# Performance work log

Measured on AMD Instinct MI355X. Metric: run time of the kernel, lower is better.

## Reference

```python
import jax, jax.numpy as jnp
import numpy as np

EPS = 1e-6
NUM_HEADS = 8
GAMMA = 0.999


def simple_rms_norm(x):
    # SimpleRMSNorm: x / ||x|| * sqrt(d) == x / sqrt(mean(x^2))
    return x * jax.lax.rsqrt(jnp.mean(x * x, axis=-1, keepdims=True) + EPS)


def setup_inputs() -> dict:
    key = jax.random.key(0)
    ks = jax.random.split(key, 12)
    B, N, M, E = 64, 14, 14, 512
    D1 = 2 * E              # expand_ratio * embed_dim = 1024
    RPE = 512               # rpe_embedding
    s = 0.02
    inp = {
        "x": jax.random.normal(ks[0], (B, N, M, E), jnp.float32),
        "H": N,
        "W": M,
        "Wu": jax.random.normal(ks[1], (E, D1), jnp.float32) * s,
        "bu": jnp.zeros((D1,), jnp.float32),
        "Wv": jax.random.normal(ks[2], (E, D1), jnp.float32) * s,
        "bv": jnp.zeros((D1,), jnp.float32),
        "Wo": jax.random.normal(ks[3], (D1, E), jnp.float32) * s,
        "bo": jnp.zeros((E,), jnp.float32),
        "rpe_pos_w": jax.random.normal(ks[4], (2, RPE), jnp.float32) * s,
        "rpe_pos_b": jnp.zeros((RPE,), jnp.float32),
        "rpe_w1": jax.random.normal(ks[5], (RPE, RPE), jnp.float32) * s,
        "rpe_b1": jnp.zeros((RPE,), jnp.float32),
        "rpe_w2": jax.random.normal(ks[6], (RPE, RPE), jnp.float32) * s,
        "rpe_b2": jnp.zeros((RPE,), jnp.float32),
        "rpe_w3": jax.random.normal(ks[7], (RPE, RPE), jnp.float32) * s,
        "rpe_b3": jnp.zeros((RPE,), jnp.float32),
        "rpe_out_w": jax.random.normal(ks[8], (RPE, D1), jnp.float32) * s,
        "rpe_out_b": jnp.zeros((D1,), jnp.float32),
    }
    return inp


def gtu2d_forward(x, Wu, bu, Wv, bv, Wo, bo,
                  rpe_pos_w, rpe_pos_b, rpe_w1, rpe_b1, rpe_w2, rpe_b2,
                  rpe_w3, rpe_b3, rpe_out_w, rpe_out_b):
    B, n, m, E = x.shape
    d1 = Wu.shape[1]
    hd = d1 // NUM_HEADS
    # dual gated projections
    u = jax.nn.silu(x @ Wu + bu)                      # (B, n, m, d1)
    v = jax.nn.silu(x @ Wv + bv)
    v = v.reshape(B, n, m, NUM_HEADS, hd).transpose(0, 3, 1, 2, 4)  # (B, h, n, m, d)

    # --- Tno2D: RPE MLP produces Toeplitz coefficients for relative positions ---
    ii = jnp.arange(-(n - 1), n, dtype=jnp.float32)
    jj = jnp.arange(-(m - 1), m, dtype=jnp.float32)
    pos = jnp.stack(jnp.meshgrid(ii, jj, indexing="ij"), axis=-1)  # (2n-1, 2m-1, 2)
    r = pos @ rpe_pos_w + rpe_pos_b
    for w, b in ((rpe_w1, rpe_b1), (rpe_w2, rpe_b2), (rpe_w3, rpe_b3)):
        r = jax.nn.relu(simple_rms_norm(r)) @ w + b
    r = jax.nn.relu(simple_rms_norm(r)) @ rpe_out_w + rpe_out_b  # (2n-1, 2m-1, h*d)
    a = r.reshape(2 * n - 1, 2 * m - 1, NUM_HEADS, hd).transpose(2, 0, 1, 3)
    # decay: gamma^(|i|+|j|)
    dist = jnp.abs(pos[..., 0]) + jnp.abs(pos[..., 1])  # (2n-1, 2m-1)
    a = a * (GAMMA ** dist)[None, :, :, None]

    # embed coefficients into circular kernel (h, 2n, 2m, d); index n / m are zero
    t = jnp.zeros((NUM_HEADS, 2 * n, 2 * m, hd), a.dtype)
    t = t.at[:, :n, :m].set(a[:, n - 1:, m - 1:])
    t = t.at[:, n + 1:, :m].set(a[:, :n - 1, m - 1:])
    t = t.at[:, :n, m + 1:].set(a[:, n - 1:, :m - 1])
    t = t.at[:, n + 1:, m + 1:].set(a[:, :n - 1, :m - 1])

    # 2D Toeplitz matvec via circular convolution / FFT
    xf = jnp.fft.rfft2(v, s=(2 * n, 2 * m), axes=(2, 3))
    tf = jnp.fft.rfft2(t, s=(2 * n, 2 * m), axes=(1, 2))
    y = jnp.fft.irfft2(xf * tf[None], s=(2 * n, 2 * m), axes=(2, 3))[:, :, :n, :m, :]
    y = y.transpose(0, 2, 3, 1, 4).reshape(B, n, m, d1)  # 'b h n m d -> b n m (h d)'

    return (u * y) @ Wo + bo


def reference(x, H, W, Wu, bu, Wv, bv, Wo, bo,
              rpe_pos_w, rpe_pos_b, rpe_w1, rpe_b1, rpe_w2, rpe_b2,
              rpe_w3, rpe_b3, rpe_out_w, rpe_out_b):
    # H, W are unused by Gtu2d.forward (spatial dims are carried by x)
    return gtu2d_forward(x, Wu, bu, Wv, bv, Wo, bo,
                         rpe_pos_w, rpe_pos_b, rpe_w1, rpe_b1, rpe_w2, rpe_b2,
                         rpe_w3, rpe_b3, rpe_out_w, rpe_out_b)
```

## Files before the change

kernel.cpp:

```cpp
#include <hip/hip_runtime.h>
#include <hip/hip_bf16.h>

typedef __hip_bfloat16 bf16;
typedef __attribute__((ext_vector_type(8))) short bf16x8;
typedef __attribute__((ext_vector_type(4))) float f32x4;

constexpr int NB    = 64;
constexpr int EE    = 512;
constexpr int RPOS  = 27 * 27;
constexpr int ROWS  = NB * 14 * 14;
constexpr int UVNWG = 392;

#define RMS_EPS 1e-6f
#define GAMMA_LOG2 (-0.00144344319f)

__device__ __forceinline__ void  stf(float* p, float v) { *p = v; }
__device__ __forceinline__ void  stf(bf16* p, float v)  { *p = __float2bfloat16(v); }

__device__ __forceinline__ void gload_lds16(const bf16* g, bf16* l) {
    __builtin_amdgcn_global_load_lds(
        (const __attribute__((address_space(1))) void*)g,
        (__attribute__((address_space(3))) void*)l, 16, 0, 0);
}

#define VMCNT(n) asm volatile("s_waitcnt vmcnt(" #n ")" ::: "memory")

__global__ __launch_bounds__(256) void k_prep(const float* __restrict__ Wu,
                                              const float* __restrict__ Wv,
                                              const float* __restrict__ Wo,
                                              const float* __restrict__ w1,
                                              const float* __restrict__ w2,
                                              const float* __restrict__ w3,
                                              const float* __restrict__ wOut,
                                              const float* __restrict__ bu,
                                              const float* __restrict__ bv,
                                              const float* __restrict__ x,
                                              const float* __restrict__ rpw,
                                              const float* __restrict__ rpb,
                                              bf16* __restrict__ WuvT,
                                              bf16* __restrict__ WoT,
                                              bf16* __restrict__ w1T,
                                              bf16* __restrict__ w2T,
                                              bf16* __restrict__ w3T,
                                              bf16* __restrict__ wOutT,
                                              float* __restrict__ biasUv,
                                              bf16* __restrict__ xb,
                                              bf16* __restrict__ rnA) {
    __shared__ float t[32][33];
    __shared__ float ps[4];
    const int tid = threadIdx.x;
    int b = blockIdx.x;

    const float* src = nullptr; bf16* dst = nullptr; int R = 0, C = 0, nbx = 0;
    if (b < 512)        { src = Wu;   dst = WuvT;                      R = 512;  C = 1024; nbx = 32; }
    else if (b < 1024)  { b -= 512;   src = Wv; dst = WuvT + (size_t)1024 * 512; R = 512; C = 1024; nbx = 32; }
    else if (b < 1536)  { b -= 1024;  src = Wo;   dst = WoT;           R = 1024; C = 512;  nbx = 16; }
    else if (b < 1792)  { b -= 1536;  src = w1;   dst = w1T;           R = 512;  C = 512;  nbx = 16; }
    else if (b < 2048)  { b -= 1792;  src = w2;   dst = w2T;           R = 512;  C = 512;  nbx = 16; }
    else if (b < 2304)  { b -= 2048;  src = w3;   dst = w3T;           R = 512;  C = 512;  nbx = 16; }
    else if (b < 2816)  { b -= 2304;  src = wOut; dst = wOutT;         R = 512;  C = 1024; nbx = 32; }
    else if (b < 2824) {
        int c = (b - 2816) * 256 + tid;
        if (c < 2048) biasUv[c] = (c < 1024) ? bu[c] : bv[c - 1024];
        return;
    } else if (b < 9096) {
        int i = (b - 2824) * 256 + tid;
        float4 v = *(const float4*)&x[(size_t)i * 4];
        bf16* d = &xb[(size_t)i * 4];
        d[0] = __float2bfloat16(v.x);
        d[1] = __float2bfloat16(v.y);
        d[2] = __float2bfloat16(v.z);
        d[3] = __float2bfloat16(v.w);
        return;
    } else {
        int p = b - 9096;
        float ii = (float)(p / 27 - 13);
        float jj = (float)(p % 27 - 13);
        int c0 = tid, c1 = tid + 256;
        float v0 = ii * rpw[c0] + jj * rpw[512 + c0] + rpb[c0];
        float v1 = ii * rpw[c1] + jj * rpw[512 + c1] + rpb[c1];
        float s = v0 * v0 + v1 * v1;
        #pragma unroll
        for (int off = 32; off; off >>= 1) s += __shfl_down(s, off, 64);
        if ((tid & 63) == 0) ps[tid >> 6] = s;
        __syncthreads();
        float tot = ps[0] + ps[1] + ps[2] + ps[3];
        float scale = rsqrtf(tot * (1.0f / 512.0f) + RMS_EPS);
        rnA[(size_t)p * 512 + c0] = __float2bfloat16(fmaxf(v0 * scale, 0.0f));
        rnA[(size_t)p * 512 + c1] = __float2bfloat16(fmaxf(v1 * scale, 0.0f));
        return;
    }
    int bx = (b % nbx) * 32;
    int by = (b / nbx) * 32;
    int tx = tid & 31, ty = tid >> 5;
    #pragma unroll
    for (int i = 0; i < 4; ++i)
        t[ty + i * 8][tx] = src[(size_t)(by + ty + i * 8) * C + bx + tx];
    __syncthreads();
    #pragma unroll
    for (int i = 0; i < 4; ++i)
        dst[(size_t)(bx + ty + i * 8) * R + by + tx] = __float2bfloat16(t[tx][ty + i * 8]);
}

template <int SCALE_IN, int EPI>
__device__ __forceinline__ void rpe_body(const bf16* __restrict__ A,
                                         const bf16* __restrict__ Bt,
                                         const float* __restrict__ bias,
                                         const float* __restrict__ pIn,
                                         float* __restrict__ pOut,
                                         bf16* __restrict__ out,
                                         int bx, int by, int M, int N, int K,
                                         bf16* As, bf16* Bs, int tid) {
    const int m0 = by * 64;
    const int n0 = bx * 64;
    const int lane = tid & 63;
    const int w = (tid >> 6) & 3;
    const int lr = lane & 15;
    const int lk = (lane >> 4) * 8;
    const int row = tid >> 2;
    const int seg = (tid & 3) * 8;

    f32x4 acc[4] = {};
    const int KT = K >> 5;

    gload_lds16(&A[(size_t)(m0 + row) * K + seg], &As[tid * 8]);
    gload_lds16(&Bt[(size_t)(n0 + row) * K + seg], &Bs[tid * 8]);
    for (int t = 0; t < KT; ++t) {
        const int d = t & 1;
        if (t + 1 < KT) {
            gload_lds16(&A[(size_t)(m0 + row) * K + (t + 1) * 32 + seg], &As[(d ^ 1) * 2048 + tid * 8]);
            gload_lds16(&Bt[(size_t)(n0 + row) * K + (t + 1) * 32 + seg], &Bs[(d ^ 1) * 2048 + tid * 8]);
            VMCNT(2);
        } else {
            VMCNT(0);
        }
        __builtin_amdgcn_s_barrier();
        __builtin_amdgcn_sched_barrier(0);
        bf16x8 af = *(const bf16x8*)&As[d * 2048 + (w * 16 + lr) * 32 + lk];
        #pragma unroll
        for (int j = 0; j < 4; ++j) {
            bf16x8 bf = *(const bf16x8*)&Bs[d * 2048 + (j * 16 + lr) * 32 + lk];
            acc[j] = __builtin_amdgcn_mfma_f32_16x16x32_bf16(af, bf, acc[j], 0, 0, 0);
        }
        __builtin_amdgcn_s_barrier();
    }

    const int crow = (lane >> 4) * 4;
    const int ccol = lane & 15;
    float sc[4];
    #pragma unroll
    for (int r = 0; r < 4; ++r) {
        sc[r] = 1.0f;
        if (SCALE_IN) {
            int gr = m0 + w * 16 + crow + r;
            if (gr < M) {
                const float* pp = &pIn[(size_t)gr * 8];
                float s8 = pp[0] + pp[1] + pp[2] + pp[3] + pp[4] + pp[5] + pp[6] + pp[7];
                sc[r] = rsqrtf(s8 * (1.0f / 512.0f) + RMS_EPS);
            }
        }
    }
    float rowsq[4] = {0.f, 0.f, 0.f, 0.f};
    #pragma unroll
    for (int j = 0; j < 4; ++j) {
        int gc = n0 + j * 16 + ccol;
        float bb = bias[gc];
        #pragma unroll
        for (int r = 0; r < 4; ++r) {
            int gr = m0 + w * 16 + crow + r;
            float val = acc[j][r] * sc[r] + bb;
            if (EPI == 0) {
                rowsq[r] += val * val;
                if (gr < M) out[(size_t)gr * N + gc] = __float2bfloat16(fmaxf(val, 0.0f));
            } else {
                if (gr < M) {
                    int i = gr / 27, jj = gr % 27;
                    float decay = exp2f((float)(abs(i - 13) + abs(jj - 13)) * GAMMA_LOG2);
                    out[(size_t)gr * N + gc] = __float2bfloat16(val * decay);
                }
            }
        }
    }
    if (EPI == 0) {
        #pragma unroll
        for (int r = 0; r < 4; ++r) {
            #pragma unroll
            for (int m = 1; m < 16; m <<= 1) rowsq[r] += __shfl_xor(rowsq[r], m, 64);
        }
        if ((lane & 15) == 0) {
            #pragma unroll
            for (int r = 0; r < 4; ++r) {
                int gr = m0 + w * 16 + crow + r;
                if (gr < M) pOut[(size_t)gr * 8 + bx] = rowsq[r];
            }
        }
    }
}

template <int SCALE_IN, int EPI>
__global__ __launch_bounds__(256) void k_rpe_gemm(const bf16* __restrict__ A,
                                                  const bf16* __restrict__ Bt,
                                                  const float* __restrict__ bias,
                                                  const float* __restrict__ pIn,
                                                  float* __restrict__ pOut,
                                                  bf16* __restrict__ out,
                                                  int M, int N, int K) {
    __shared__ bf16 As[2][2048];
    __shared__ bf16 Bs[2][2048];
    rpe_body<SCALE_IN, EPI>(A, Bt, bias, pIn, pOut, out,
                            blockIdx.x, blockIdx.y, M, N, K,
                            &As[0][0], &Bs[0][0], threadIdx.x);
}

template <int EPI, typename TO>
__global__ __launch_bounds__(256) void k_mgemm(const bf16* __restrict__ A, int lda,
                                               const bf16* __restrict__ Bt,
                                               const float* __restrict__ bias,
                                               TO* __restrict__ out, int ldo,
                                               int M, int N, int K) {
    __shared__ bf16 As[128 * 32];
    __shared__ bf16 Bs[128 * 32];
    const int tid = threadIdx.x;
    const int m0 = blockIdx.y * 128;
    const int n0 = blockIdx.x * 128;
    const int lane = tid & 63;
    const int w = tid >> 6;
    const int wr = (w >> 1) * 64;
    const int wc = (w & 1) * 64;
    const int lr = lane & 15;
    const int lk = (lane >> 4) * 8;

    f32x4 acc[4][4] = {};

    for (int k0 = 0; k0 < K; k0 += 32) {
        #pragma unroll
        for (int t = 0; t < 2; ++t) {
            int flat = t * 256 + tid;
            int row = flat >> 2;
            int seg = (flat & 3) * 8;
            gload_lds16(&A[(size_t)(m0 + row) * lda + k0 + seg], &As[flat * 8]);
            gload_lds16(&Bt[(size_t)(n0 + row) * K + k0 + seg], &Bs[flat * 8]);
        }
        __syncthreads();
        bf16x8 af[4], bf[4];
        #pragma unroll
        for (int i = 0; i < 4; ++i) {
            af[i] = *(const bf16x8*)&As[(wr + i * 16 + lr) * 32 + lk];
            bf[i] = *(const bf16x8*)&Bs[(wc + i * 16 + lr) * 32 + lk];
        }
        #pragma unroll
        for (int i = 0; i < 4; ++i)
            #pragma unroll
            for (int j = 0; j < 4; ++j)
                acc[i][j] = __builtin_amdgcn_mfma_f32_16x16x32_bf16(af[i], bf[j], acc[i][j], 0, 0, 0);
        __syncthreads();
    }

    const int crow = (lane >> 4) * 4;
    const int ccol = lane & 15;
    #pragma unroll
    for (int i = 0; i < 4; ++i)
        #pragma unroll
        for (int j = 0; j < 4; ++j) {
            int gc = n0 + wc + j * 16 + ccol;
            float bb = bias[gc];
            #pragma unroll
            for (int r = 0; r < 4; ++r) {
                int gr = m0 + wr + i * 16 + crow + r;
                float val = acc[i][j][r] + bb;
                if (EPI == 1) val = val / (1.0f + expf(-val));
                stf(&out[(size_t)gr * ldo + gc], val);
            }
        }
}

__global__ __launch_bounds__(512, 2) void k_uv_l1(const bf16* __restrict__ A, int lda,
                                                  const bf16* __restrict__ Bt,
                                                  const float* __restrict__ bias,
                                                  bf16* __restrict__ out, int ldo,
                                                  int nb ,
                                                  const bf16* __restrict__ rA,
                                                  const bf16* __restrict__ w1T,
                                                  const float* __restrict__ b1,
                                                  float* __restrict__ p1,
                                                  bf16* __restrict__ rB) {
    constexpr int KT = 8;
    constexpr int K = KT * 64;
    __shared__ __align__(16) char lds[131072];

    const int tid = threadIdx.x;

    if (blockIdx.x >= UVNWG) {
        const int orig = (blockIdx.x - UVNWG) * 2 + (tid >> 8);
        const int half = tid >> 8;
        bf16* As = (bf16*)(lds + half * 32768);
        bf16* Bs = (bf16*)(lds + half * 32768 + 8192);
        rpe_body<0, 0>(rA, w1T, b1, nullptr, p1, rB,
                       orig & 7, orig >> 3, RPOS, 512, 512, As, Bs, tid & 255);
        return;
    }

    const int lane = tid & 63;
    const int wid = tid >> 6;
    const int wr = wid >> 2;
    const int wc = wid & 3;

    int wgid = blockIdx.x;
    {
        int cpx = UVNWG >> 3;
        wgid = (wgid & 7) * cpx + (wgid >> 3);
    }
    const int m0 = (wgid / nb) * 256;
    const int n0 = (wgid % nb) * 256;

    auto ldsA = [&](int d, int kh) -> char* { return (char*)lds + d * 32768 + kh * 16384; };
    auto ldsB = [&](int d, int kh) -> char* { return (char*)lds + 65536 + d * 32768 + kh * 16384; };

    auto stage = [&](int op, int kh, int tt) {
        char* base = op ? ldsB(tt & 1, kh) : ldsA(tt & 1, kh);
        const bf16* g = op ? Bt : A;
        const int rowbase = op ? n0 : m0;
        const int ldr = op ? K : lda;
        #pragma unroll
        for (int l = 0; l < 2; ++l) {
            int q = tid + l * 512;
            int r = q >> 2;
            int cl = (q & 3) ^ ((r ^ (r >> 2)) & 3);
            const bf16* src = g + (size_t)(rowbase + r) * ldr + tt * 64 + kh * 32 + cl * 8;
            gload_lds16(src, (bf16*)(base + q * 16));
        }
    };
    auto rdA = [&](int d, int ks, int mi) -> bf16x8 {
        int row = wr * 128 + mi * 16 + (lane & 15);
        int ch = (lane >> 4) ^ ((row ^ (row >> 2)) & 3);
        return *(const bf16x8*)(ldsA(d, ks) + row * 64 + ch * 16);
    };
    auto rdB = [&](int d, int ks, int nj) -> bf16x8 {
        int row = wc * 64 + nj * 16 + (lane & 15);
        int ch = (lane >> 4) ^ ((row ^ (row >> 2)) & 3);
        return *(const bf16x8*)(ldsB(d, ks) + row * 64 + ch * 16);
    };

    f32x4 acc[8][4] = {};
    bf16x8 aF[4], bF[4];

    stage(0, 0, 0); stage(1, 0, 0); stage(0, 1, 0); stage(1, 1, 0);
    stage(0, 0, 1); stage(1, 0, 1);
    VMCNT(8);
    __builtin_amdgcn_s_barrier();
    __builtin_amdgcn_sched_barrier(0);

    #pragma unroll
    for (int t = 0; t < KT; ++t) {
        const int d = t & 1;
        #pragma unroll
        for (int mi = 0; mi < 4; ++mi) aF[mi] = rdA(d, 0, mi);
        #pragma unroll
        for (int nj = 0; nj < 4; ++nj) bF[nj] = rdB(d, 0, nj);
        if (t + 1 < KT) stage(0, 1, t + 1);
        __builtin_amdgcn_s_barrier();
        __builtin_amdgcn_s_setprio(1);
        #pragma unroll
        for (int mi = 0; mi < 4; ++mi)
            #pragma unroll
            for (int nj = 0; nj < 4; ++nj)
                acc[mi][nj] = __builtin_amdgcn_mfma_f32_16x16x32_bf16(aF[mi], bF[nj], acc[mi][nj], 0, 0, 0);
        __builtin_amdgcn_s_setprio(0);
        __builtin_amdgcn_s_barrier();
        #pragma unroll
        for (int mi = 0; mi < 4; ++mi) aF[mi] = rdA(d, 0, mi + 4);
        if (t + 1 < KT) stage(1, 1, t + 1);
        if (t + 1 < KT) { VMCNT(8); } else { VMCNT(0); }
        __builtin_amdgcn_s_barrier();
        __builtin_amdgcn_sched_barrier(0);
        __builtin_amdgcn_s_setprio(1);
        #pragma unroll
        for (int mi = 0; mi < 4; ++mi)
            #pragma unroll
            for (int nj = 0; nj < 4; ++nj)
                acc[mi + 4][nj] = __builtin_amdgcn_mfma_f32_16x16x32_bf16(aF[mi], bF[nj], acc[mi + 4][nj], 0, 0, 0);
        __builtin_amdgcn_s_setprio(0);
        __builtin_amdgcn_s_barrier();
        #pragma unroll
        for (int mi = 0; mi < 4; ++mi) aF[mi] = rdA(d, 1, mi);
        #pragma unroll
        for (int nj = 0; nj < 4; ++nj) bF[nj] = rdB(d, 1, nj);
        if (t + 2 < KT) stage(0, 0, t + 2);
        __builtin_amdgcn_s_barrier();
        __builtin_amdgcn_s_setprio(1);
        #pragma unroll
        for (int mi = 0; mi < 4; ++mi)
            #pragma unroll
            for (int nj = 0; nj < 4; ++nj)
                acc[mi][nj] = __builtin_amdgcn_mfma_f32_16x16x32_bf16(aF[mi], bF[nj], acc[mi][nj], 0, 0, 0);
        __builtin_amdgcn_s_setprio(0);
        __builtin_amdgcn_s_barrier();
        #pragma unroll
        for (int mi = 0; mi < 4; ++mi) aF[mi] = rdA(d, 1, mi + 4);
        if (t + 2 < KT) stage(1, 0, t + 2);
        if (t + 2 < KT)      { VMCNT(8); }
        else if (t + 1 < KT) { VMCNT(4); }
        __builtin_amdgcn_s_barrier();
        __builtin_amdgcn_sched_barrier(0);
        __builtin_amdgcn_s_setprio(1);
        #pragma unroll
        for (int mi = 0; mi < 4; ++mi)
            #pragma unroll
            for (int nj = 0; nj < 4; ++nj)
                acc[mi + 4][nj] = __builtin_amdgcn_mfma_f32_16x16x32_bf16(aF[mi], bF[nj], acc[mi + 4][nj], 0, 0, 0);
        __builtin_amdgcn_s_setprio(0);
        __builtin_amdgcn_s_barrier();
    }

    const int crow = (lane >> 4) * 4;
    const int ccol = lane & 15;
    #pragma unroll
    for (int mi = 0; mi < 8; ++mi)
        #pragma unroll
        for (int nj = 0; nj < 4; ++nj) {
            int gc = n0 + wc * 64 + nj * 16 + ccol;
            float bb = bias[gc];
            #pragma unroll
            for (int r = 0; r < 4; ++r) {
                int gr = m0 + wr * 128 + mi * 16 + crow + r;
                float val = acc[mi][nj][r] + bb;
                val = val / (1.0f + expf(-val));
                stf(&out[(size_t)gr * ldo + gc], val);
            }
        }
}

__global__ __launch_bounds__(256) void k_vt_l2(const bf16* __restrict__ uv,
                                               bf16* __restrict__ Vt,
                                               const bf16* __restrict__ rB,
                                               const bf16* __restrict__ w2T,
                                               const float* __restrict__ b2,
                                               const float* __restrict__ p1,
                                               float* __restrict__ p2,
                                               bf16* __restrict__ rA) {
    __shared__ __align__(16) char lraw[25872 > 16384 ? 25872 : 16384];
    const int tid = threadIdx.x;

    if (blockIdx.x >= 1024) {
        const int orig = blockIdx.x - 1024;
        bf16* As = (bf16*)lraw;
        bf16* Bs = (bf16*)(lraw + 8192);
        rpe_body<1, 0>(rB, w2T, b2, p1, p2, rA,
                       orig & 7, orig >> 3, RPOS, 512, 512, As, Bs, tid);
        return;
    }

    typedef bf16 row66[66];
    row66* t = (row66*)lraw;
    const int c0 = (blockIdx.x & 15) * 64;
    const int b  = blockIdx.x >> 4;
    for (int f = tid; f < 196 * 64; f += 256) {
        int ij = f >> 6, cl = f & 63;
        t[ij][cl] = uv[((size_t)b * 196 + ij) * 2048 + 1024 + c0 + cl];
    }
    __syncthreads();
    const bf16 z = __float2bfloat16(0.0f);
    for (int f = tid; f < 64 * 224; f += 256) {
        int cl = f / 224, ij = f - cl * 224;
        Vt[((size_t)(c0 + cl) * 64 + b) * 224 + ij] = (ij < 196) ? t[ij][cl] : z;
    }
}

__global__ __launch_bounds__(256) void k_convm(const bf16* __restrict__ Ab,
                                               const bf16* __restrict__ Vt,
                                               bf16* __restrict__ Yt) {
    __shared__ __align__(16) bf16 Ts[112 * 232];
    __shared__ bf16 As[736];
    const int mh = blockIdx.x;
    const int cl = blockIdx.y;
    const int c = (int)blockIdx.z * 512 + cl;
    const int tid = threadIdx.x;
    const int mbase = mh * 112;

    for (int e = tid; e < 729; e += 256)
        As[e] = Ab[(size_t)e * 1024 + c];
    __syncthreads();

    const bf16 z = __float2bfloat16(0.0f);
    if (tid < 224) {
        const int i = tid / 14, j = tid - i * 14;
        const bool kvalid = tid < 196;
        int p = mbase / 14, q = 0;
        for (int r = 0; r < 112; ++r) {
            bf16 val = z;
            if (kvalid && (mbase + r) < 196)
                val = As[(p - i + 13) * 27 + (q - j + 13)];
            Ts[r * 232 + tid] = val;
            if (++q == 14) { q = 0; ++p; }
        }
    }
    __syncthreads();

    const int lane = tid & 63;
    const int w = tid >> 6;
    const int lr = lane & 15;
    const int lk = (lane >> 4) * 8;
    const bf16* Vc = Vt + (size_t)c * 64 * 224;

    bf16x8 bfr[7];
    #pragma unroll
    for (int ks = 0; ks < 7; ++ks)
        bfr[ks] = *(const bf16x8*)&Vc[(size_t)(w * 16 + lr) * 224 + ks * 32 + lk];

    f32x4 acc[7] = {};
    #pragma unroll
    for (int ks = 0; ks < 7; ++ks)
        #pragma unroll
        for (int mi = 0; mi < 7; ++mi) {
            bf16x8 a = *(const bf16x8*)&Ts[(mi * 16 + lr) * 232 + ks * 32 + lk];
            acc[mi] = __builtin_amdgcn_mfma_f32_16x16x32_bf16(a, bfr[ks], acc[mi], 0, 0, 0);
        }

    const int crow = (lane >> 4) * 4;
    const int bb = w * 16 + (lane & 15);
    #pragma unroll
    for (int mi = 0; mi < 7; ++mi) {
        int pq = mbase + mi * 16 + crow;
        #pragma unroll
        for (int r = 0; r < 4; ++r)
            if (pq + r < 196)
                Yt[((size_t)c * 196 + pq + r) * 64 + bb] = __float2bfloat16(acc[mi][r]);
    }
}

__global__ __launch_bounds__(256) void k_gate(bf16* __restrict__ uv,
                                              const bf16* __restrict__ Yt) {
    const int pq = blockIdx.x;
    const int ct = blockIdx.y;
    const int cb = (int)blockIdx.z * 512;
    const int tid = threadIdx.x;
    __shared__ float t[64][65];
    for (int f = tid; f < 64 * 64; f += 256) {
        int cr = f >> 6, bcol = f & 63;
        t[cr][bcol] = __bfloat162float(Yt[((size_t)(cb + ct * 64 + cr) * 196 + pq) * 64 + bcol]);
    }
    __syncthreads();
    for (int f = tid; f < 64 * 64; f += 256) {
        int br = f >> 6, cc = f & 63;
        size_t row = (size_t)br * 196 + pq;
        int cglob = cb + ct * 64 + cc;
        float uu = __bfloat162float(uv[row * 2048 + cglob]);
        uv[row * 2048 + 1024 + cglob] = __float2bfloat16(t[cc][br] * uu);
    }
}

extern "C" void kernel_launch(void* const* d_in, const int* in_sizes, int n_in,
                              void* d_out, int out_size, void* d_ws, size_t ws_size,
                              hipStream_t stream) {
    const float* x    = (const float*)d_in[0];
    const float* Wu   = (const float*)d_in[3];
    const float* bu   = (const float*)d_in[4];
    const float* Wv   = (const float*)d_in[5];
    const float* bv   = (const float*)d_in[6];
    const float* Wo   = (const float*)d_in[7];
    const float* bo   = (const float*)d_in[8];
    const float* rpw  = (const float*)d_in[9];
    const float* rpb  = (const float*)d_in[10];
    const float* w1   = (const float*)d_in[11];
    const float* b1   = (const float*)d_in[12];
    const float* w2   = (const float*)d_in[13];
    const float* b2   = (const float*)d_in[14];
    const float* w3   = (const float*)d_in[15];
    const float* b3   = (const float*)d_in[16];
    const float* wOut = (const float*)d_in[17];
    const float* bOut = (const float*)d_in[18];

    char* ws = (char*)d_ws;
    size_t off = 0;
    auto take = [&](size_t bytes) { char* p = ws + off; off += (bytes + 255) & ~size_t(255); return p; };
    bf16*  rnA    = (bf16*)take((size_t)768 * 512 * 2);
    bf16*  rnB    = (bf16*)take((size_t)768 * 512 * 2);
    float* p1     = (float*)take((size_t)768 * 8 * 4);
    float* p2     = (float*)take((size_t)768 * 8 * 4);
    float* p3     = (float*)take((size_t)768 * 8 * 4);
    bf16*  Ab     = (bf16*)take((size_t)RPOS * 1024 * 2);
    bf16*  xb     = (bf16*)take((size_t)ROWS * EE * 2);
    bf16*  WuvT   = (bf16*)take((size_t)2048 * 512 * 2);
    bf16*  WoT    = (bf16*)take((size_t)512 * 1024 * 2);
    bf16*  w1T    = (bf16*)take((size_t)512 * 512 * 2);
    bf16*  w2T    = (bf16*)take((size_t)512 * 512 * 2);
    bf16*  w3T    = (bf16*)take((size_t)512 * 512 * 2);
    bf16*  wOutT  = (bf16*)take((size_t)1024 * 512 * 2);
    float* biasUv = (float*)take(2048 * 4);
    bf16*  uvb    = (bf16*)take((size_t)ROWS * 2048 * 2);
    bf16*  Vt     = (bf16*)take((size_t)1024 * 64 * 224 * 2);
    bf16*  Yt     = (bf16*)take((size_t)1024 * 196 * 64 * 2);

    k_prep<<<9825, 256, 0, stream>>>(Wu, Wv, Wo, w1, w2, w3, wOut, bu, bv, x,
                                     rpw, rpb,
                                     WuvT, WoT, w1T, w2T, w3T, wOutT, biasUv, xb, rnA);

    k_uv_l1<<<UVNWG + 48, 512, 0, stream>>>(xb, 512, WuvT, biasUv, uvb, 2048, 8,
                                            rnA, w1T, b1, p1, rnB);

    k_vt_l2<<<1120, 256, 0, stream>>>(uvb, Vt, rnB, w2T, b2, p1, p2, rnA);

    k_rpe_gemm<1, 0><<<dim3(8, 12), 256, 0, stream>>>(rnA, w3T, b3, p2, p3, rnB, RPOS, 512, 512);
    k_rpe_gemm<1, 2><<<dim3(16, 12), 256, 0, stream>>>(rnB, wOutT, bOut, p3, nullptr, Ab, RPOS, 1024, 512);

    k_convm<<<dim3(2, 512, 2), 256, 0, stream>>>(Ab, Vt, Yt);
    k_gate<<<dim3(196, 8, 2), 256, 0, stream>>>(uvb, Yt);

    k_mgemm<0, float><<<dim3(4, 98), 256, 0, stream>>>(uvb + 1024, 2048, WoT, bo,
                                                       (float*)d_out, 512, ROWS, 512, 1024);
}
```

Measured before the change: 198.3 us.

## Split V transpose across two launches co-scheduled with RPE layers 2 and 3

The V-transpose work is split into two halves by batch. Each half is fused with one RPE MLP layer (layer 2 and then layer 3), which removes the standalone layer-3 RPE GEMM launch and lets the small RPE GEMMs overlap with the memory-bound transpose. Separately, the conv kernel now processes both 112-row halves in one block, loading the Toeplitz coefficients and V fragments once instead of twice. This halves the grid and adds an extra barrier round per block, which reduces parallelism in exchange for reuse.

```diff
diff --git a/kernel.cpp b/kernel.cpp
--- a/kernel.cpp
+++ b/kernel.cpp
@@ -430,22 +430,22 @@
         }
 }
 
-__global__ __launch_bounds__(256) void k_vt_l2(const bf16* __restrict__ uv,
-                                               bf16* __restrict__ Vt,
-                                               const bf16* __restrict__ rB,
-                                               const bf16* __restrict__ w2T,
-                                               const float* __restrict__ b2,
-                                               const float* __restrict__ p1,
-                                               float* __restrict__ p2,
-                                               bf16* __restrict__ rA) {
-    __shared__ __align__(16) char lraw[25872 > 16384 ? 25872 : 16384];
+__global__ __launch_bounds__(256) void k_vt_rpe(const bf16* __restrict__ uv,
+                                                bf16* __restrict__ Vt, int bbase,
+                                                const bf16* __restrict__ rIn,
+                                                const bf16* __restrict__ wT,
+                                                const float* __restrict__ bias,
+                                                const float* __restrict__ pIn,
+                                                float* __restrict__ pOut,
+                                                bf16* __restrict__ rOut) {
+    __shared__ __align__(16) char lraw[25872];
     const int tid = threadIdx.x;
 
-    if (blockIdx.x >= 1024) {
-        const int orig = blockIdx.x - 1024;
+    if (blockIdx.x >= 512) {
+        const int orig = blockIdx.x - 512;
         bf16* As = (bf16*)lraw;
         bf16* Bs = (bf16*)(lraw + 8192);
-        rpe_body<1, 0>(rB, w2T, b2, p1, p2, rA,
+        rpe_body<1, 0>(rIn, wT, bias, pIn, pOut, rOut,
                        orig & 7, orig >> 3, RPOS, 512, 512, As, Bs, tid);
         return;
     }
@@ -453,7 +453,7 @@
     typedef bf16 row66[66];
     row66* t = (row66*)lraw;
     const int c0 = (blockIdx.x & 15) * 64;
-    const int b  = blockIdx.x >> 4;
+    const int b  = bbase + (blockIdx.x >> 4);
     for (int f = tid; f < 196 * 64; f += 256) {
         int ij = f >> 6, cl = f & 63;
         t[ij][cl] = uv[((size_t)b * 196 + ij) * 2048 + 1024 + c0 + cl];
@@ -471,30 +471,12 @@
                                                bf16* __restrict__ Yt) {
     __shared__ __align__(16) bf16 Ts[112 * 232];
     __shared__ bf16 As[736];
-    const int mh = blockIdx.x;
-    const int cl = blockIdx.y;
-    const int c = (int)blockIdx.z * 512 + cl;
+    const int cl = blockIdx.x;
+    const int c = (int)blockIdx.y * 512 + cl;
     const int tid = threadIdx.x;
-    const int mbase = mh * 112;
 
     for (int e = tid; e < 729; e += 256)
         As[e] = Ab[(size_t)e * 1024 + c];
-    __syncthreads();
-
-    const bf16 z = __float2bfloat16(0.0f);
-    if (tid < 224) {
-        const int i = tid / 14, j = tid - i * 14;
-        const bool kvalid = tid < 196;
-        int p = mbase / 14, q = 0;
-        for (int r = 0; r < 112; ++r) {
-            bf16 val = z;
-            if (kvalid && (mbase + r) < 196)
-                val = As[(p - i + 13) * 27 + (q - j + 13)];
-            Ts[r * 232 + tid] = val;
-            if (++q == 14) { q = 0; ++p; }
-        }
-    }
-    __syncthreads();
 
     const int lane = tid & 63;
     const int w = tid >> 6;
@@ -507,24 +489,47 @@
     for (int ks = 0; ks < 7; ++ks)
         bfr[ks] = *(const bf16x8*)&Vc[(size_t)(w * 16 + lr) * 224 + ks * 32 + lk];
 
-    f32x4 acc[7] = {};
-    #pragma unroll
-    for (int ks = 0; ks < 7; ++ks)
-        #pragma unroll
-        for (int mi = 0; mi < 7; ++mi) {
-            bf16x8 a = *(const bf16x8*)&Ts[(mi * 16 + lr) * 232 + ks * 32 + lk];
-            acc[mi] = __builtin_amdgcn_mfma_f32_16x16x32_bf16(a, bfr[ks], acc[mi], 0, 0, 0);
-        }
-
+    __syncthreads();
+
+    const bf16 z = __float2bfloat16(0.0f);
     const int crow = (lane >> 4) * 4;
     const int bb = w * 16 + (lane & 15);
-    #pragma unroll
-    for (int mi = 0; mi < 7; ++mi) {
-        int pq = mbase + mi * 16 + crow;
-        #pragma unroll
-        for (int r = 0; r < 4; ++r)
-            if (pq + r < 196)
-                Yt[((size_t)c * 196 + pq + r) * 64 + bb] = __float2bfloat16(acc[mi][r]);
+
+    #pragma unroll
+    for (int mh = 0; mh < 2; ++mh) {
+        const int mbase = mh * 112;
+        if (tid < 224) {
+            const int i = tid / 14, j = tid - i * 14;
+            const bool kvalid = tid < 196;
+            int p = mbase / 14, q = 0;
+            for (int r = 0; r < 112; ++r) {
+                bf16 val = z;
+                if (kvalid && (mbase + r) < 196)
+                    val = As[(p - i + 13) * 27 + (q - j + 13)];
+                Ts[r * 232 + tid] = val;
+                if (++q == 14) { q = 0; ++p; }
+            }
+        }
+        __syncthreads();
+
+        f32x4 acc[7] = {};
+        #pragma unroll
+        for (int ks = 0; ks < 7; ++ks)
+            #pragma unroll
+            for (int mi = 0; mi < 7; ++mi) {
+                bf16x8 a = *(const bf16x8*)&Ts[(mi * 16 + lr) * 232 + ks * 32 + lk];
+                acc[mi] = __builtin_amdgcn_mfma_f32_16x16x32_bf16(a, bfr[ks], acc[mi], 0, 0, 0);
+            }
+
+        #pragma unroll
+        for (int mi = 0; mi < 7; ++mi) {
+            int pq = mbase + mi * 16 + crow;
+            #pragma unroll
+            for (int r = 0; r < 4; ++r)
+                if (pq + r < 196)
+                    Yt[((size_t)c * 196 + pq + r) * 64 + bb] = __float2bfloat16(acc[mi][r]);
+        }
+        __syncthreads();
     }
 }
 
@@ -598,12 +603,13 @@
     k_uv_l1<<<UVNWG + 48, 512, 0, stream>>>(xb, 512, WuvT, biasUv, uvb, 2048, 8,
                                             rnA, w1T, b1, p1, rnB);
 
-    k_vt_l2<<<1120, 256, 0, stream>>>(uvb, Vt, rnB, w2T, b2, p1, p2, rnA);
-
-    k_rpe_gemm<1, 0><<<dim3(8, 12), 256, 0, stream>>>(rnA, w3T, b3, p2, p3, rnB, RPOS, 512, 512);
+    k_vt_rpe<<<608, 256, 0, stream>>>(uvb, Vt, 0,  rnB, w2T, b2, p1, p2, rnA);
+    k_vt_rpe<<<608, 256, 0, stream>>>(uvb, Vt, 32, rnA, w3T, b3, p2, p3, rnB);
+
     k_rpe_gemm<1, 2><<<dim3(16, 12), 256, 0, stream>>>(rnB, wOutT, bOut, p3, nullptr, Ab, RPOS, 1024, 512);
 
-    k_convm<<<dim3(2, 512, 2), 256, 0, stream>>>(Ab, Vt, Yt);
+    k_convm<<<dim3(512, 2), 256, 0, stream>>>(Ab, Vt, Yt);
+
     k_gate<<<dim3(196, 8, 2), 256, 0, stream>>>(uvb, Yt);
 
     k_mgemm<0, float><<<dim3(4, 98), 256, 0, stream>>>(uvb + 1024, 2048, WoT, bo,
```

Result: faster. 192.0 us (-3.2%).
